# Performance work log

Hardware: AMD Instinct MI355X
Metric: run time of the kernel (lower is better)

The kernel has to match this reference:

```python
import jax, jax.numpy as jnp
import numpy as np

N_NODES = 100000
N_EDGES = 3200000
F_IN, F_HID, F_OUT = 32, 32, 16


def spline_conv(x, edge_index, edge_attr, W, root, bias):
    """SplineConv, dim=1, kernel_size=2, degree=1, open spline, aggr='mean'.
    Basis weights over the 2 kernel slots are (1-u, u) for pseudo u in [0,1).
    W: [2, Fin, Fout], root: [Fin, Fout], bias: [Fout]."""
    src, dst = edge_index[0], edge_index[1]
    u = jnp.clip(edge_attr[:, 0:1], 0.0, 1.0)          # [E,1]
    x_src = x[src]                                      # [E,Fin] gather
    msg = (1.0 - u) * (x_src @ W[0]) + u * (x_src @ W[1])  # [E,Fout]
    agg = jax.ops.segment_sum(msg, dst, num_segments=x.shape[0])
    cnt = jax.ops.segment_sum(jnp.ones((msg.shape[0],), dtype=x.dtype), dst,
                              num_segments=x.shape[0])
    agg = agg / jnp.maximum(cnt, 1.0)[:, None]          # mean aggregation
    return agg + x @ root + bias


def setup_inputs() -> dict:
    key = jax.random.key(0)
    ks = jax.random.split(key, 9)
    x = jax.random.normal(ks[0], (N_NODES, F_IN), dtype=jnp.float32)
    edge_index = jax.random.randint(ks[1], (2, N_EDGES), 0, N_NODES, dtype=jnp.int64)
    edge_attr = jax.random.uniform(ks[2], (N_EDGES, 1), dtype=jnp.float32)
    s1 = 1.0 / np.sqrt(F_IN)
    s2 = 1.0 / np.sqrt(F_HID)
    W1 = jax.random.normal(ks[3], (2, F_IN, F_HID), dtype=jnp.float32) * s1
    root1 = jax.random.normal(ks[4], (F_IN, F_HID), dtype=jnp.float32) * s1
    b1 = jnp.zeros((F_HID,), dtype=jnp.float32)
    W2 = jax.random.normal(ks[5], (2, F_HID, F_OUT), dtype=jnp.float32) * s2
    root2 = jax.random.normal(ks[6], (F_HID, F_OUT), dtype=jnp.float32) * s2
    b2 = jnp.zeros((F_OUT,), dtype=jnp.float32)
    return {"x": x, "edge_index": edge_index, "edge_attr": edge_attr,
            "W1": W1, "root1": root1, "b1": b1,
            "W2": W2, "root2": root2, "b2": b2}


def reference(x, edge_index, edge_attr, W1, root1, b1, W2, root2, b2):
    # dropout is identity in eval mode
    h = jax.nn.relu(spline_conv(x, edge_index, edge_attr, W1, root1, b1))
    h = spline_conv(h, edge_index, edge_attr, W2, root2, b2)
    return jax.nn.log_softmax(h, axis=1)
```

## Files before the change

### kernel.cpp

```cpp
#include <hip/hip_runtime.h>
#include <math.h>

#define NN 100000
#define NE 3200000
#define BSH 6
#define BSZ 64
#define NBKT 1563
#define CAP 2560
#define STILE 8192
#define NTBS 391
#define NPB 1563
#define TST 68
#define NOFF (NBKT + 1)
#define OS2W 392

#define FMA4(a, s, v) { (a).x += (s)*(v).x; (a).y += (s)*(v).y; (a).z += (s)*(v).z; (a).w += (s)*(v).w; }

typedef float v2f __attribute__((ext_vector_type(2)));

__device__ __forceinline__ unsigned fp8pack4(float a, float b, float c, float d) {
    int r = __builtin_amdgcn_cvt_pk_fp8_f32(a, b, 0, false);
    r = __builtin_amdgcn_cvt_pk_fp8_f32(c, d, r, true);
    return (unsigned)r;
}

#define LDE(pp, vv, idx) { int e_ = (idx); \
    if (e_ < cn) { pp = (unsigned)pks[cs + e_]; vv = x1[(size_t)(pp >> 15) * 8 + j]; } \
    else { pp = 0u; vv = 0u; } }
#define ACC(pp, vv) { float u_ = (float)((pp) & 511u) * (1.f / 511.f); \
    v2f lo_ = __builtin_amdgcn_cvt_pk_f32_fp8((vv), false); \
    v2f hi_ = __builtin_amdgcn_cvt_pk_f32_fp8((vv), true); \
    T0 += lo_.x; B0 += u_ * lo_.x;  T1 += lo_.y; B1 += u_ * lo_.y; \
    T2 += hi_.x; B2 += u_ * hi_.x;  T3 += hi_.y; B3 += u_ * hi_.y; }

__global__ __launch_bounds__(512, 6) void sp_k(
    const int* __restrict__ ei, const float* __restrict__ ea,
    const float* __restrict__ x, const float* __restrict__ R, const float* __restrict__ b,
    int* __restrict__ pk, unsigned short* __restrict__ offs,
    unsigned* __restrict__ xb, float* __restrict__ xr)
{
    __shared__ __align__(16) union {
        struct { int h[2048]; int staged[STILE]; } sc;
        struct { float Rs[1024]; float xs[64 * 33]; } pp;
    } sm;
    int t = threadIdx.x;

    if (blockIdx.x < NTBS) {
        int* h = sm.sc.h;
        for (int i = t; i < 2048; i += 512) h[i] = 0;
        __syncthreads();
        int e0 = blockIdx.x * STILE;
        int cntblk = NE - e0; if (cntblk > STILE) cntblk = STILE;
        unsigned pck[16]; int bk[16];
        #pragma unroll
        for (int i = 0; i < 16; i++) {
            int e = e0 + i * 512 + t;
            bk[i] = -1;
            if (e < NE) {
                int s = ei[e];
                int d = ei[NE + e];
                float u = fminf(fmaxf(ea[e], 0.f), 1.f);
                unsigned uq = __float2uint_rn(u * 511.f);
                bk[i] = d >> BSH;
                pck[i] = ((unsigned)s << 15) | ((unsigned)(d & (BSZ - 1)) << 9) | uq;
                atomicAdd(&h[bk[i]], 1);
            }
        }
        __syncthreads();
        int4 hc = ((const int4*)h)[t];
        int s4 = hc.x + hc.y + hc.z + hc.w;
        int lane = t & 63, wv = t >> 6;
        int inc = s4;
        #pragma unroll
        for (int ofs = 1; ofs < 64; ofs <<= 1) {
            int v = __shfl_up(inc, ofs);
            if (lane >= ofs) inc += v;
        }
        int* wsum = sm.sc.staged;
        if (lane == 63) wsum[wv] = inc;
        __syncthreads();
        int base = 0;
        #pragma unroll
        for (int i = 0; i < 8; i++) { int v = wsum[i]; if (i < wv) base += v; }
        int ex = base + inc - s4;
        ((int4*)h)[t] = make_int4(ex, ex + hc.x, ex + hc.x + hc.y, ex + hc.x + hc.y + hc.z);
        __syncthreads();
        for (int k = t; k < NOFF; k += 512)
            offs[(size_t)blockIdx.x * NOFF + k] = (unsigned short)h[k];
        __syncthreads();
        #pragma unroll
        for (int i = 0; i < 16; i++) {
            if (bk[i] >= 0) {
                int pos = atomicAdd(&h[bk[i]], 1);
                sm.sc.staged[pos] = (int)pck[i];
            }
        }
        __syncthreads();
        int* seg = pk + (size_t)blockIdx.x * STILE;
        for (int i = t; i * 4 < cntblk; i += 512)
            ((int4*)seg)[i] = ((const int4*)sm.sc.staged)[i];
    } else {
        for (int i = t; i < 1024; i += 512) sm.pp.Rs[i] = R[i];
        int nb = (blockIdx.x - NTBS) * 64;
        for (int i = t; i < 2048; i += 512) {
            int n = nb + (i >> 5);
            sm.pp.xs[(i >> 5) * 33 + (i & 31)] = (n < NN) ? x[n * 32 + (i & 31)] : 0.f;
        }
        __syncthreads();
        int local = t >> 3, c = t & 7;
        int n = nb + local;
        float4 a2 = make_float4(0.f, 0.f, 0.f, 0.f);
        #pragma unroll
        for (int k = 0; k < 32; k++) {
            float xk = sm.pp.xs[local * 33 + k];
            float4 r = ((const float4*)sm.pp.Rs)[k * 8 + c];
            FMA4(a2, xk, r);
        }
        if (n < NN) {
            float4 bb = ((const float4*)b)[c];
            a2.x += bb.x; a2.y += bb.y; a2.z += bb.z; a2.w += bb.w;
            ((float4*)xr)[n * 8 + c] = a2;
            xb[n * 8 + c] = fp8pack4(sm.pp.xs[local * 33 + c * 4 + 0],
                                     sm.pp.xs[local * 33 + c * 4 + 1],
                                     sm.pp.xs[local * 33 + c * 4 + 2],
                                     sm.pp.xs[local * 33 + c * 4 + 3]);
        }
    }
}

__global__ __launch_bounds__(256) void tr_k(
    const unsigned short* __restrict__ offs, unsigned* __restrict__ offs2)
{
    __shared__ unsigned short st[64][68];
    int kt = blockIdx.x % 25;
    int tt = blockIdx.x / 25;
    int t = threadIdx.x;
    for (int i = t; i < 64 * 66; i += 256) {
        int r = i / 66, c = i % 66;
        int row = tt * 64 + r, k = kt * 64 + c;
        st[r][c] = (row < NTBS && k < NOFF) ? offs[(size_t)row * NOFF + k] : (unsigned short)0;
    }
    __syncthreads();
    for (int i = t; i < 64 * 64; i += 256) {
        int kl = i >> 6, tl = i & 63;
        int k = kt * 64 + kl, row = tt * 64 + tl;
        if (k < NBKT && row < NTBS) {
            unsigned o0 = st[tl][kl];
            unsigned cnt = (unsigned)st[tl][kl + 1] - o0;
            offs2[(size_t)k * OS2W + row] = o0 | (cnt << 16);
        }
    }
}

__global__ __launch_bounds__(512, 6) void agg1_k(
    const int* __restrict__ pk, const unsigned* __restrict__ offs2,
    const unsigned* __restrict__ xb, const float* __restrict__ W,
    const float* __restrict__ R2, const float* __restrict__ b2,
    const float* __restrict__ xr, unsigned* __restrict__ hb, float* __restrict__ hr,
    int* __restrict__ pk2, int* __restrict__ cnt2)
{
    __shared__ float Wc[2048];
    __shared__ float R2s[512];
    __shared__ int ccnt[BSZ], coff[BSZ];
    __shared__ int wsum[8];
    __shared__ __align__(16) char smraw[BSZ * TST * 4];
    __shared__ __align__(16) union { int staged[CAP]; float hs[BSZ * 33]; } su;
    int* pks = (int*)smraw;
    float* tb = (float*)smraw;

    int t = threadIdx.x;
    for (int i = t; i < 1024; i += 512) {
        float w0 = W[i];
        Wc[i] = w0;
        Wc[1024 + i] = W[1024 + i] - w0;
    }
    if (t < 512) R2s[t] = R2[t];
    if (t < BSZ) ccnt[t] = 0;

    int bkt = blockIdx.x;
    int cnt = 0, o0 = 0;
    if (t < NTBS) {
        unsigned pc = offs2[(size_t)bkt * OS2W + t];
        o0 = (int)(pc & 0xFFFFu);
        cnt = (int)(pc >> 16);
    }
    int lane = t & 63, wv = t >> 6;
    int inc = cnt;
    #pragma unroll
    for (int ofs = 1; ofs < 64; ofs <<= 1) {
        int v = __shfl_up(inc, ofs);
        if (lane >= ofs) inc += v;
    }
    if (lane == 63) wsum[wv] = inc;
    __syncthreads();
    int base = 0, tot = 0;
    #pragma unroll
    for (int i = 0; i < 8; i++) { int v = wsum[i]; tot += v; if (i < wv) base += v; }
    int dst = base + inc - cnt;
    int ne = tot < CAP ? tot : CAP;
    if (dst + cnt > CAP) { cnt = CAP - dst; if (cnt < 0) cnt = 0; }
    const int* seg = pk + (size_t)t * STILE + o0;
    int i2 = 0;
    for (; i2 + 4 <= cnt; i2 += 4) {
        int v0 = seg[i2], v1 = seg[i2 + 1], v2 = seg[i2 + 2], v3 = seg[i2 + 3];
        su.staged[dst + i2] = v0; su.staged[dst + i2 + 1] = v1;
        su.staged[dst + i2 + 2] = v2; su.staged[dst + i2 + 3] = v3;
    }
    for (; i2 < cnt; i2++) su.staged[dst + i2] = seg[i2];
    __syncthreads();

    unsigned er[5]; int rk[5];
    #pragma unroll
    for (int i = 0; i < 5; i++) {
        int e = i * 512 + t;
        rk[i] = -1;
        if (e < ne) {
            er[i] = (unsigned)su.staged[e];
            rk[i] = atomicAdd(&ccnt[(er[i] >> 9) & (BSZ - 1)], 1);
        }
    }
    __syncthreads();
    if (t < BSZ) {
        int v = ccnt[t], sc = v;
        #pragma unroll
        for (int ofs = 1; ofs < 64; ofs <<= 1) {
            int nn = __shfl_up(sc, ofs);
            if (t >= ofs) sc += nn;
        }
        coff[t] = sc - v;
    }
    __syncthreads();
    #pragma unroll
    for (int i = 0; i < 5; i++)
        if (rk[i] >= 0) pks[coff[(er[i] >> 9) & (BSZ - 1)] + rk[i]] = (int)er[i];
    if (t < BSZ) cnt2[bkt * BSZ + t] = ccnt[t];
    __syncthreads();

    {
        int n4 = (ne + 3) >> 2;
        int4* dp = (int4*)(pk2 + (size_t)bkt * CAP);
        for (int i = t; i < n4; i += 512) dp[i] = ((const int4*)pks)[i];
    }

    int r = t >> 3, j = t & 7;
    int cs = coff[r], cn = ccnt[r];
    const unsigned* x1 = xb;
    float T0=0,T1=0,T2=0,T3=0,B0=0,B1=0,B2=0,B3=0;
    unsigned pa0, pa1, pa2, pa3, pb0, pb1, pb2, pb3;
    unsigned va0, va1, va2, va3, vb0, vb1, vb2, vb3;
    LDE(pa0, va0, 0) LDE(pa1, va1, 1) LDE(pa2, va2, 2) LDE(pa3, va3, 3)
    LDE(pb0, vb0, 4) LDE(pb1, vb1, 5) LDE(pb2, vb2, 6) LDE(pb3, vb3, 7)
    for (int k = 0; k < cn; k += 8) {
        ACC(pa0, va0) ACC(pa1, va1) ACC(pa2, va2) ACC(pa3, va3)
        LDE(pa0, va0, k + 8)  LDE(pa1, va1, k + 9)  LDE(pa2, va2, k + 10) LDE(pa3, va3, k + 11)
        ACC(pb0, vb0) ACC(pb1, vb1) ACC(pb2, vb2) ACC(pb3, vb3)
        LDE(pb0, vb0, k + 12) LDE(pb1, vb1, k + 13) LDE(pb2, vb2, k + 14) LDE(pb3, vb3, k + 15)
    }
    __syncthreads();

    ((float4*)(tb + r * TST + 4 * j))[0]      = make_float4(T0, T1, T2, T3);
    ((float4*)(tb + r * TST + 32 + 4 * j))[0] = make_float4(B0, B1, B2, B3);
    __syncthreads();

    {
        int row = t >> 3, cc = t & 7;
        int n = bkt * BSZ + row;
        float inv = 1.f / fmaxf((float)ccnt[row], 1.f);
        float4 acc = make_float4(0.f, 0.f, 0.f, 0.f);
        #pragma unroll
        for (int k = 0; k < 32; k++) {
            float sa = tb[row * TST + k];
            float4 w = ((const float4*)Wc)[k * 8 + cc];
            FMA4(acc, sa, w);
        }
        #pragma unroll
        for (int k = 0; k < 32; k++) {
            float sb = tb[row * TST + 32 + k];
            float4 w = ((const float4*)Wc)[(32 + k) * 8 + cc];
            FMA4(acc, sb, w);
        }
        float h0 = 0.f, h1 = 0.f, h2 = 0.f, h3 = 0.f;
        if (n < NN) {
            float4 rr = ((const float4*)xr)[n * 8 + cc];
            h0 = fmaxf(acc.x * inv + rr.x, 0.f);
            h1 = fmaxf(acc.y * inv + rr.y, 0.f);
            h2 = fmaxf(acc.z * inv + rr.z, 0.f);
            h3 = fmaxf(acc.w * inv + rr.w, 0.f);
            hb[n * 8 + cc] = fp8pack4(h0, h1, h2, h3);
        }
        su.hs[row * 33 + cc * 4 + 0] = h0;
        su.hs[row * 33 + cc * 4 + 1] = h1;
        su.hs[row * 33 + cc * 4 + 2] = h2;
        su.hs[row * 33 + cc * 4 + 3] = h3;
    }
    __syncthreads();

    #pragma unroll
    for (int p = 0; p < 2; p++) {
        int idx = p * 512 + t;
        int row = idx >> 4, f = idx & 15;
        int n = bkt * BSZ + row;
        if (n < NN) {
            float o = 0.f;
            #pragma unroll
            for (int k = 0; k < 32; k++) o += su.hs[row * 33 + k] * R2s[k * 16 + f];
            hr[n * 16 + f] = o + b2[f];
        }
    }
}

__global__ __launch_bounds__(512, 8) void agg2_k(
    const int* __restrict__ pk2, const int* __restrict__ cnt2,
    const unsigned* __restrict__ hb, const float* __restrict__ W,
    const float* __restrict__ hr, float* __restrict__ out)
{
    __shared__ float Wc[1024];
    __shared__ int ccnt[BSZ], coff[BSZ];
    __shared__ int smne;
    __shared__ __align__(16) char smraw[BSZ * TST * 4];
    int* pks = (int*)smraw;
    float* tb = (float*)smraw;

    int t = threadIdx.x;
    if (t < 512) {
        float w0 = W[t];
        Wc[t] = w0;
        Wc[512 + t] = W[512 + t] - w0;
    }
    int bkt = blockIdx.x;
    if (t < BSZ) {
        int v = cnt2[bkt * BSZ + t];
        ccnt[t] = v;
        int sc = v;
        #pragma unroll
        for (int ofs = 1; ofs < 64; ofs <<= 1) {
            int nn = __shfl_up(sc, ofs);
            if (t >= ofs) sc += nn;
        }
        coff[t] = sc - v;
        if (t == 63) smne = sc;
    }
    __syncthreads();
    int ne = smne; if (ne > CAP) ne = CAP;
    {
        int n4 = (ne + 3) >> 2;
        const int4* sp4 = (const int4*)(pk2 + (size_t)bkt * CAP);
        for (int i = t; i < n4; i += 512) ((int4*)pks)[i] = sp4[i];
    }
    __syncthreads();

    int r = t >> 3, j = t & 7;
    int cs = coff[r], cn = ccnt[r];
    const unsigned* x1 = hb;
    float T0=0,T1=0,T2=0,T3=0,B0=0,B1=0,B2=0,B3=0;
    unsigned pa0, pa1, pa2, pa3, pb0, pb1, pb2, pb3;
    unsigned va0, va1, va2, va3, vb0, vb1, vb2, vb3;
    LDE(pa0, va0, 0) LDE(pa1, va1, 1) LDE(pa2, va2, 2) LDE(pa3, va3, 3)
    LDE(pb0, vb0, 4) LDE(pb1, vb1, 5) LDE(pb2, vb2, 6) LDE(pb3, vb3, 7)
    for (int k = 0; k < cn; k += 8) {
        ACC(pa0, va0) ACC(pa1, va1) ACC(pa2, va2) ACC(pa3, va3)
        LDE(pa0, va0, k + 8)  LDE(pa1, va1, k + 9)  LDE(pa2, va2, k + 10) LDE(pa3, va3, k + 11)
        ACC(pb0, vb0) ACC(pb1, vb1) ACC(pb2, vb2) ACC(pb3, vb3)
        LDE(pb0, vb0, k + 12) LDE(pb1, vb1, k + 13) LDE(pb2, vb2, k + 14) LDE(pb3, vb3, k + 15)
    }
    __syncthreads();

    ((float4*)(tb + r * TST + 4 * j))[0]      = make_float4(T0, T1, T2, T3);
    ((float4*)(tb + r * TST + 32 + 4 * j))[0] = make_float4(B0, B1, B2, B3);
    __syncthreads();

    #pragma unroll
    for (int p = 0; p < 2; p++) {
        int row = p * 32 + (t >> 4), f = t & 15;
        int n = bkt * BSZ + row;
        float inv = 1.f / fmaxf((float)ccnt[row], 1.f);
        float o = 0.f;
        #pragma unroll
        for (int k = 0; k < 32; k++) o += tb[row * TST + k] * Wc[k * 16 + f];
        #pragma unroll
        for (int k = 0; k < 32; k++) o += tb[row * TST + 32 + k] * Wc[(32 + k) * 16 + f];
        if (n < NN) {
            o = o * inv + hr[n * 16 + f];
            float m = o;
            #pragma unroll
            for (int ofs = 8; ofs; ofs >>= 1) m = fmaxf(m, __shfl_xor(m, ofs, 16));
            float sm = expf(o - m);
            #pragma unroll
            for (int ofs = 8; ofs; ofs >>= 1) sm += __shfl_xor(sm, ofs, 16);
            out[n * 16 + f] = o - (m + logf(sm));
        }
    }
}

extern "C" void kernel_launch(void* const* d_in, const int* in_sizes, int n_in,
                              void* d_out, int out_size, void* d_ws, size_t ws_size,
                              hipStream_t stream) {
    const float* x     = (const float*)d_in[0];
    const int*   ei    = (const int*)d_in[1];
    const float* ea    = (const float*)d_in[2];
    const float* W1    = (const float*)d_in[3];
    const float* root1 = (const float*)d_in[4];
    const float* b1    = (const float*)d_in[5];
    const float* W2    = (const float*)d_in[6];
    const float* root2 = (const float*)d_in[7];
    const float* b2    = (const float*)d_in[8];
    float* out = (float*)d_out;

    int* ws = (int*)d_ws;
    int* pk = ws;
    size_t o_offs  = NE;
    size_t o_offs2 = o_offs + 305764;
    size_t o_pk2   = o_offs2 + (size_t)NBKT * OS2W;
    size_t o_cnt2  = o_pk2 + (size_t)NBKT * CAP;
    size_t o_xb    = o_cnt2 + (size_t)NBKT * BSZ;
    size_t o_hb    = o_xb + (size_t)NN * 8;
    size_t o_xr    = o_hb + (size_t)NN * 8;
    size_t o_hr    = o_xr + (size_t)NN * 32;

    unsigned short* offs = (unsigned short*)(ws + o_offs);
    unsigned* offs2 = (unsigned*)(ws + o_offs2);
    int* pk2 = ws + o_pk2;
    int* cnt2 = ws + o_cnt2;
    unsigned* xb = (unsigned*)(ws + o_xb);
    unsigned* hb = (unsigned*)(ws + o_hb);
    float* xr = (float*)(ws + o_xr);
    float* hr = (float*)(ws + o_hr);

    sp_k   <<<NTBS + NPB, 512, 0, stream>>>(ei, ea, x, root1, b1, pk, offs, xb, xr);
    tr_k   <<<25 * 7, 256, 0, stream>>>(offs, offs2);
    agg1_k <<<NBKT, 512, 0, stream>>>(pk, offs2, xb, W1, root2, b2, xr, hb, hr, pk2, cnt2);
    agg2_k <<<NBKT, 512, 0, stream>>>(pk2, cnt2, hb, W2, hr, out);
}
```

Measured before the change: 226.6 us.

## Split edge bucketing into two-level radix pass with dedicated partition kernel

```diff
diff --git a/kernel.cpp b/kernel.cpp
--- a/kernel.cpp
+++ b/kernel.cpp
@@ -3,16 +3,18 @@
 
 #define NN 100000
 #define NE 3200000
-#define BSH 6
 #define BSZ 64
 #define NBKT 1563
+#define NBKT2 1564
 #define CAP 2560
 #define STILE 8192
 #define NTBS 391
 #define NPB 1563
 #define TST 68
-#define NOFF (NBKT + 1)
-#define OS2W 392
+#define NSUP 391
+#define NOFA (NSUP + 1)
+#define OSBW 392
+#define SCAP 9216
 
 #define FMA4(a, s, v) { (a).x += (s)*(v).x; (a).y += (s)*(v).y; (a).z += (s)*(v).z; (a).w += (s)*(v).w; }
 
@@ -33,72 +35,95 @@
     T0 += lo_.x; B0 += u_ * lo_.x;  T1 += lo_.y; B1 += u_ * lo_.y; \
     T2 += hi_.x; B2 += u_ * hi_.x;  T3 += hi_.y; B3 += u_ * hi_.y; }
 
+#define WALK_BODY() \
+    int r = t >> 3, j = t & 7; \
+    int cs = coff[r], cn = ccnt[r]; \
+    float T0=0,T1=0,T2=0,T3=0,B0=0,B1=0,B2=0,B3=0; \
+    unsigned pa0, pa1, pa2, pa3, pb0, pb1, pb2, pb3; \
+    unsigned va0, va1, va2, va3, vb0, vb1, vb2, vb3; \
+    LDE(pa0, va0, 0) LDE(pa1, va1, 1) LDE(pa2, va2, 2) LDE(pa3, va3, 3) \
+    LDE(pb0, vb0, 4) LDE(pb1, vb1, 5) LDE(pb2, vb2, 6) LDE(pb3, vb3, 7) \
+    for (int k = 0; k < cn; k += 8) { \
+        ACC(pa0, va0) ACC(pa1, va1) ACC(pa2, va2) ACC(pa3, va3) \
+        LDE(pa0, va0, k + 8)  LDE(pa1, va1, k + 9)  LDE(pa2, va2, k + 10) LDE(pa3, va3, k + 11) \
+        ACC(pb0, vb0) ACC(pb1, vb1) ACC(pb2, vb2) ACC(pb3, vb3) \
+        LDE(pb0, vb0, k + 12) LDE(pb1, vb1, k + 13) LDE(pb2, vb2, k + 14) LDE(pb3, vb3, k + 15) \
+    } \
+    __syncthreads();                       \
+    ((float4*)(tb + r * TST + 4 * j))[0]      = make_float4(T0, T1, T2, T3); \
+    ((float4*)(tb + r * TST + 32 + 4 * j))[0] = make_float4(B0, B1, B2, B3); \
+    __syncthreads();
+
 __global__ __launch_bounds__(512, 6) void sp_k(
     const int* __restrict__ ei, const float* __restrict__ ea,
     const float* __restrict__ x, const float* __restrict__ R, const float* __restrict__ b,
-    int* __restrict__ pk, unsigned short* __restrict__ offs,
+    int* __restrict__ pkA, unsigned char* __restrict__ idxA, unsigned short* __restrict__ offsA,
     unsigned* __restrict__ xb, float* __restrict__ xr)
 {
     __shared__ __align__(16) union {
-        struct { int h[2048]; int staged[STILE]; } sc;
+        struct { int h[NSUP + 1]; int wsum[8]; int staged[STILE]; char sidx[STILE]; } sc;
         struct { float Rs[1024]; float xs[64 * 33]; } pp;
     } sm;
     int t = threadIdx.x;
 
     if (blockIdx.x < NTBS) {
         int* h = sm.sc.h;
-        for (int i = t; i < 2048; i += 512) h[i] = 0;
+        if (t < NSUP) h[t] = 0;
         __syncthreads();
         int e0 = blockIdx.x * STILE;
         int cntblk = NE - e0; if (cntblk > STILE) cntblk = STILE;
-        unsigned pck[16]; int bk[16];
+        unsigned pck[16]; int key[16];
         #pragma unroll
         for (int i = 0; i < 16; i++) {
             int e = e0 + i * 512 + t;
-            bk[i] = -1;
+            key[i] = -1;
             if (e < NE) {
                 int s = ei[e];
                 int d = ei[NE + e];
                 float u = fminf(fmaxf(ea[e], 0.f), 1.f);
                 unsigned uq = __float2uint_rn(u * 511.f);
-                bk[i] = d >> BSH;
-                pck[i] = ((unsigned)s << 15) | ((unsigned)(d & (BSZ - 1)) << 9) | uq;
-                atomicAdd(&h[bk[i]], 1);
+                key[i] = d >> 6;
+                pck[i] = ((unsigned)s << 15) | ((unsigned)(d & 63) << 9) | uq;
+                atomicAdd(&h[key[i] >> 2], 1);
             }
         }
         __syncthreads();
-        int4 hc = ((const int4*)h)[t];
-        int s4 = hc.x + hc.y + hc.z + hc.w;
+        int cb = (t < NSUP) ? h[t] : 0;
         int lane = t & 63, wv = t >> 6;
-        int inc = s4;
+        int inc = cb;
         #pragma unroll
         for (int ofs = 1; ofs < 64; ofs <<= 1) {
             int v = __shfl_up(inc, ofs);
             if (lane >= ofs) inc += v;
         }
-        int* wsum = sm.sc.staged;
-        if (lane == 63) wsum[wv] = inc;
+        if (lane == 63) sm.sc.wsum[wv] = inc;
         __syncthreads();
         int base = 0;
         #pragma unroll
-        for (int i = 0; i < 8; i++) { int v = wsum[i]; if (i < wv) base += v; }
-        int ex = base + inc - s4;
-        ((int4*)h)[t] = make_int4(ex, ex + hc.x, ex + hc.x + hc.y, ex + hc.x + hc.y + hc.z);
-        __syncthreads();
-        for (int k = t; k < NOFF; k += 512)
-            offs[(size_t)blockIdx.x * NOFF + k] = (unsigned short)h[k];
+        for (int i = 0; i < 8; i++) { int v = sm.sc.wsum[i]; if (i < wv) base += v; }
+        int ex = base + inc - cb;
+        __syncthreads();
+        if (t < NSUP) {
+            h[t] = ex;
+            offsA[(size_t)blockIdx.x * NOFA + t] = (unsigned short)ex;
+        }
+        if (t == 0) offsA[(size_t)blockIdx.x * NOFA + NSUP] = (unsigned short)cntblk;
         __syncthreads();
         #pragma unroll
         for (int i = 0; i < 16; i++) {
-            if (bk[i] >= 0) {
-                int pos = atomicAdd(&h[bk[i]], 1);
+            if (key[i] >= 0) {
+                int pos = atomicAdd(&h[key[i] >> 2], 1);
                 sm.sc.staged[pos] = (int)pck[i];
+                sm.sc.sidx[pos] = (char)(key[i] & 3);
             }
         }
         __syncthreads();
-        int* seg = pk + (size_t)blockIdx.x * STILE;
+        int* segA = pkA + (size_t)blockIdx.x * STILE;
         for (int i = t; i * 4 < cntblk; i += 512)
-            ((int4*)seg)[i] = ((const int4*)sm.sc.staged)[i];
+            ((int4*)segA)[i] = ((const int4*)sm.sc.staged)[i];
+        int4* segI = (int4*)(idxA + (size_t)blockIdx.x * STILE);
+        for (int i = t; i * 16 < cntblk; i += 512)
+            segI[i] = ((const int4*)sm.sc.sidx)[i];
     } else {
         for (int i = t; i < 1024; i += 512) sm.pp.Rs[i] = R[i];
         int nb = (blockIdx.x - NTBS) * 64;
@@ -129,42 +154,108 @@
 }
 
 __global__ __launch_bounds__(256) void tr_k(
-    const unsigned short* __restrict__ offs, unsigned* __restrict__ offs2)
+    const unsigned short* __restrict__ offsA, unsigned* __restrict__ offsB)
 {
     __shared__ unsigned short st[64][68];
-    int kt = blockIdx.x % 25;
-    int tt = blockIdx.x / 25;
+    int kt = blockIdx.x % 7;
+    int tt = blockIdx.x / 7;
     int t = threadIdx.x;
     for (int i = t; i < 64 * 66; i += 256) {
         int r = i / 66, c = i % 66;
         int row = tt * 64 + r, k = kt * 64 + c;
-        st[r][c] = (row < NTBS && k < NOFF) ? offs[(size_t)row * NOFF + k] : (unsigned short)0;
+        st[r][c] = (row < NTBS && k < NOFA) ? offsA[(size_t)row * NOFA + k] : (unsigned short)0;
     }
     __syncthreads();
     for (int i = t; i < 64 * 64; i += 256) {
         int kl = i >> 6, tl = i & 63;
-        int k = kt * 64 + kl, row = tt * 64 + tl;
-        if (k < NBKT && row < NTBS) {
+        int s = kt * 64 + kl, row = tt * 64 + tl;
+        if (s < NSUP && row < NTBS) {
             unsigned o0 = st[tl][kl];
             unsigned cnt = (unsigned)st[tl][kl + 1] - o0;
-            offs2[(size_t)k * OS2W + row] = o0 | (cnt << 16);
+            offsB[(size_t)s * OSBW + row] = o0 | (cnt << 16);
+        }
+    }
+}
+
+__global__ __launch_bounds__(512, 6) void pb_k(
+    const int* __restrict__ pkA, const unsigned char* __restrict__ idxA,
+    const unsigned* __restrict__ offsB,
+    int* __restrict__ pk2, int* __restrict__ cnt2)
+{
+    __shared__ int hist[256], cur[256], off[257], wsumB[8];
+    __shared__ __align__(16) int stagedB[SCAP];
+    int t = threadIdx.x;
+    int s = blockIdx.x;
+
+    int o0 = 0, cnt = 0;
+    if (t < NTBS) {
+        unsigned pc = offsB[(size_t)s * OSBW + t];
+        o0 = (int)(pc & 0xFFFFu);
+        cnt = (int)(pc >> 16);
+    }
+    if (t < 256) hist[t] = 0;
+    __syncthreads();
+
+    const int* segR = pkA + (size_t)t * STILE + o0;
+    const unsigned char* segI = idxA + (size_t)t * STILE + o0;
+    for (int i = 0; i < cnt; i++) {
+        int d9 = (int)segI[i] * 64 + ((segR[i] >> 9) & 63);
+        atomicAdd(&hist[d9], 1);
+    }
+    __syncthreads();
+
+    int cb = (t < 256) ? hist[t] : 0;
+    int lane = t & 63, wv = t >> 6;
+    int inc = cb;
+    #pragma unroll
+    for (int ofs = 1; ofs < 64; ofs <<= 1) {
+        int v = __shfl_up(inc, ofs);
+        if (lane >= ofs) inc += v;
+    }
+    if (lane == 63) wsumB[wv] = inc;
+    __syncthreads();
+    int base = 0;
+    #pragma unroll
+    for (int i = 0; i < 8; i++) { int v = wsumB[i]; if (i < wv) base += v; }
+    int ex = base + inc - cb;
+    if (t < 256) { off[t] = ex; cur[t] = ex; }
+    if (t == 255) off[256] = ex + cb;
+    __syncthreads();
+
+    for (int i = 0; i < cnt; i++) {
+        int rrec = segR[i];
+        int d9 = (int)segI[i] * 64 + ((rrec >> 9) & 63);
+        int pos = atomicAdd(&cur[d9], 1);
+        if (pos < SCAP) stagedB[pos] = rrec;
+    }
+    __syncthreads();
+
+    if (t < 256) cnt2[((size_t)s * 4 + (t >> 6)) * 64 + (t & 63)] = hist[t];
+    #pragma unroll
+    for (int bq = 0; bq < 4; bq++) {
+        int bas = off[bq * 64];
+        int n = off[(bq + 1) * 64] - bas;
+        if (n > CAP) n = CAP;
+        int* dp = pk2 + (size_t)(s * 4 + bq) * CAP;
+        for (int i = t; i < n; i += 512) {
+            int p2 = bas + i;
+            if (p2 < SCAP) dp[i] = stagedB[p2];
         }
     }
 }
 
 __global__ __launch_bounds__(512, 6) void agg1_k(
-    const int* __restrict__ pk, const unsigned* __restrict__ offs2,
+    const int* __restrict__ pk2, const int* __restrict__ cnt2,
     const unsigned* __restrict__ xb, const float* __restrict__ W,
     const float* __restrict__ R2, const float* __restrict__ b2,
-    const float* __restrict__ xr, unsigned* __restrict__ hb, float* __restrict__ hr,
-    int* __restrict__ pk2, int* __restrict__ cnt2)
+    const float* __restrict__ xr, unsigned* __restrict__ hb, float* __restrict__ hr)
 {
     __shared__ float Wc[2048];
     __shared__ float R2s[512];
     __shared__ int ccnt[BSZ], coff[BSZ];
-    __shared__ int wsum[8];
+    __shared__ int smne;
     __shared__ __align__(16) char smraw[BSZ * TST * 4];
-    __shared__ __align__(16) union { int staged[CAP]; float hs[BSZ * 33]; } su;
+    __shared__ float hs[BSZ * 33];
     int* pks = (int*)smraw;
     float* tb = (float*)smraw;
 
@@ -175,92 +266,31 @@
         Wc[1024 + i] = W[1024 + i] - w0;
     }
     if (t < 512) R2s[t] = R2[t];
-    if (t < BSZ) ccnt[t] = 0;
 
     int bkt = blockIdx.x;
-    int cnt = 0, o0 = 0;
-    if (t < NTBS) {
-        unsigned pc = offs2[(size_t)bkt * OS2W + t];
-        o0 = (int)(pc & 0xFFFFu);
-        cnt = (int)(pc >> 16);
-    }
-    int lane = t & 63, wv = t >> 6;
-    int inc = cnt;
-    #pragma unroll
-    for (int ofs = 1; ofs < 64; ofs <<= 1) {
-        int v = __shfl_up(inc, ofs);
-        if (lane >= ofs) inc += v;
-    }
-    if (lane == 63) wsum[wv] = inc;
-    __syncthreads();
-    int base = 0, tot = 0;
-    #pragma unroll
-    for (int i = 0; i < 8; i++) { int v = wsum[i]; tot += v; if (i < wv) base += v; }
-    int dst = base + inc - cnt;
-    int ne = tot < CAP ? tot : CAP;
-    if (dst + cnt > CAP) { cnt = CAP - dst; if (cnt < 0) cnt = 0; }
-    const int* seg = pk + (size_t)t * STILE + o0;
-    int i2 = 0;
-    for (; i2 + 4 <= cnt; i2 += 4) {
-        int v0 = seg[i2], v1 = seg[i2 + 1], v2 = seg[i2 + 2], v3 = seg[i2 + 3];
-        su.staged[dst + i2] = v0; su.staged[dst + i2 + 1] = v1;
-        su.staged[dst + i2 + 2] = v2; su.staged[dst + i2 + 3] = v3;
-    }
-    for (; i2 < cnt; i2++) su.staged[dst + i2] = seg[i2];
-    __syncthreads();
-
-    unsigned er[5]; int rk[5];
-    #pragma unroll
-    for (int i = 0; i < 5; i++) {
-        int e = i * 512 + t;
-        rk[i] = -1;
-        if (e < ne) {
-            er[i] = (unsigned)su.staged[e];
-            rk[i] = atomicAdd(&ccnt[(er[i] >> 9) & (BSZ - 1)], 1);
-        }
-    }
-    __syncthreads();
     if (t < BSZ) {
-        int v = ccnt[t], sc = v;
+        int v = cnt2[bkt * BSZ + t];
+        ccnt[t] = v;
+        int sc = v;
         #pragma unroll
         for (int ofs = 1; ofs < 64; ofs <<= 1) {
             int nn = __shfl_up(sc, ofs);
             if (t >= ofs) sc += nn;
         }
         coff[t] = sc - v;
-    }
-    __syncthreads();
-    #pragma unroll
-    for (int i = 0; i < 5; i++)
-        if (rk[i] >= 0) pks[coff[(er[i] >> 9) & (BSZ - 1)] + rk[i]] = (int)er[i];
-    if (t < BSZ) cnt2[bkt * BSZ + t] = ccnt[t];
-    __syncthreads();
-
+        if (t == 63) smne = sc;
+    }
+    __syncthreads();
+    int ne = smne; if (ne > CAP) ne = CAP;
     {
         int n4 = (ne + 3) >> 2;
-        int4* dp = (int4*)(pk2 + (size_t)bkt * CAP);
-        for (int i = t; i < n4; i += 512) dp[i] = ((const int4*)pks)[i];
-    }
-
-    int r = t >> 3, j = t & 7;
-    int cs = coff[r], cn = ccnt[r];
+        const int4* sp4 = (const int4*)(pk2 + (size_t)bkt * CAP);
+        for (int i = t; i < n4; i += 512) ((int4*)pks)[i] = sp4[i];
+    }
+    __syncthreads();
+
     const unsigned* x1 = xb;
-    float T0=0,T1=0,T2=0,T3=0,B0=0,B1=0,B2=0,B3=0;
-    unsigned pa0, pa1, pa2, pa3, pb0, pb1, pb2, pb3;
-    unsigned va0, va1, va2, va3, vb0, vb1, vb2, vb3;
-    LDE(pa0, va0, 0) LDE(pa1, va1, 1) LDE(pa2, va2, 2) LDE(pa3, va3, 3)
-    LDE(pb0, vb0, 4) LDE(pb1, vb1, 5) LDE(pb2, vb2, 6) LDE(pb3, vb3, 7)
-    for (int k = 0; k < cn; k += 8) {
-        ACC(pa0, va0) ACC(pa1, va1) ACC(pa2, va2) ACC(pa3, va3)
-        LDE(pa0, va0, k + 8)  LDE(pa1, va1, k + 9)  LDE(pa2, va2, k + 10) LDE(pa3, va3, k + 11)
-        ACC(pb0, vb0) ACC(pb1, vb1) ACC(pb2, vb2) ACC(pb3, vb3)
-        LDE(pb0, vb0, k + 12) LDE(pb1, vb1, k + 13) LDE(pb2, vb2, k + 14) LDE(pb3, vb3, k + 15)
-    }
-    __syncthreads();
-
-    ((float4*)(tb + r * TST + 4 * j))[0]      = make_float4(T0, T1, T2, T3);
-    ((float4*)(tb + r * TST + 32 + 4 * j))[0] = make_float4(B0, B1, B2, B3);
-    __syncthreads();
+    WALK_BODY()
 
     {
         int row = t >> 3, cc = t & 7;
@@ -288,10 +318,10 @@
             h3 = fmaxf(acc.w * inv + rr.w, 0.f);
             hb[n * 8 + cc] = fp8pack4(h0, h1, h2, h3);
         }
-        su.hs[row * 33 + cc * 4 + 0] = h0;
-        su.hs[row * 33 + cc * 4 + 1] = h1;
-        su.hs[row * 33 + cc * 4 + 2] = h2;
-        su.hs[row * 33 + cc * 4 + 3] = h3;
+        hs[row * 33 + cc * 4 + 0] = h0;
+        hs[row * 33 + cc * 4 + 1] = h1;
+        hs[row * 33 + cc * 4 + 2] = h2;
+        hs[row * 33 + cc * 4 + 3] = h3;
     }
     __syncthreads();
 
@@ -303,13 +333,13 @@
         if (n < NN) {
             float o = 0.f;
             #pragma unroll
-            for (int k = 0; k < 32; k++) o += su.hs[row * 33 + k] * R2s[k * 16 + f];
+            for (int k = 0; k < 32; k++) o += hs[row * 33 + k] * R2s[k * 16 + f];
             hr[n * 16 + f] = o + b2[f];
         }
     }
 }
 
-__global__ __launch_bounds__(512, 8) void agg2_k(
+__global__ __launch_bounds__(512, 6) void agg2_k(
     const int* __restrict__ pk2, const int* __restrict__ cnt2,
     const unsigned* __restrict__ hb, const float* __restrict__ W,
     const float* __restrict__ hr, float* __restrict__ out)
@@ -349,25 +379,8 @@
     }
     __syncthreads();
 
-    int r = t >> 3, j = t & 7;
-    int cs = coff[r], cn = ccnt[r];
     const unsigned* x1 = hb;
-    float T0=0,T1=0,T2=0,T3=0,B0=0,B1=0,B2=0,B3=0;
-    unsigned pa0, pa1, pa2, pa3, pb0, pb1, pb2, pb3;
-    unsigned va0, va1, va2, va3, vb0, vb1, vb2, vb3;
-    LDE(pa0, va0, 0) LDE(pa1, va1, 1) LDE(pa2, va2, 2) LDE(pa3, va3, 3)
-    LDE(pb0, vb0, 4) LDE(pb1, vb1, 5) LDE(pb2, vb2, 6) LDE(pb3, vb3, 7)
-    for (int k = 0; k < cn; k += 8) {
-        ACC(pa0, va0) ACC(pa1, va1) ACC(pa2, va2) ACC(pa3, va3)
-        LDE(pa0, va0, k + 8)  LDE(pa1, va1, k + 9)  LDE(pa2, va2, k + 10) LDE(pa3, va3, k + 11)
-        ACC(pb0, vb0) ACC(pb1, vb1) ACC(pb2, vb2) ACC(pb3, vb3)
-        LDE(pb0, vb0, k + 12) LDE(pb1, vb1, k + 13) LDE(pb2, vb2, k + 14) LDE(pb3, vb3, k + 15)
-    }
-    __syncthreads();
-
-    ((float4*)(tb + r * TST + 4 * j))[0]      = make_float4(T0, T1, T2, T3);
-    ((float4*)(tb + r * TST + 32 + 4 * j))[0] = make_float4(B0, B1, B2, B3);
-    __syncthreads();
+    WALK_BODY()
 
     #pragma unroll
     for (int p = 0; p < 2; p++) {
@@ -407,18 +420,21 @@
     float* out = (float*)d_out;
 
     int* ws = (int*)d_ws;
-    int* pk = ws;
-    size_t o_offs  = NE;
-    size_t o_offs2 = o_offs + 305764;
-    size_t o_pk2   = o_offs2 + (size_t)NBKT * OS2W;
-    size_t o_cnt2  = o_pk2 + (size_t)NBKT * CAP;
-    size_t o_xb    = o_cnt2 + (size_t)NBKT * BSZ;
+    size_t o_pkA   = 0;
+    size_t o_idxA  = o_pkA + (size_t)NTBS * STILE;
+    size_t o_offsA = o_idxA + (size_t)NTBS * STILE / 4;
+    size_t o_offsB = o_offsA + 76640;
+    size_t o_pk2   = o_offsB + (size_t)NSUP * OSBW;
+    size_t o_cnt2  = o_pk2 + (size_t)NBKT2 * CAP;
+    size_t o_xb    = o_cnt2 + (size_t)NBKT2 * 64;
     size_t o_hb    = o_xb + (size_t)NN * 8;
     size_t o_xr    = o_hb + (size_t)NN * 8;
     size_t o_hr    = o_xr + (size_t)NN * 32;
 
-    unsigned short* offs = (unsigned short*)(ws + o_offs);
-    unsigned* offs2 = (unsigned*)(ws + o_offs2);
+    int* pkA = ws + o_pkA;
+    unsigned char* idxA = (unsigned char*)(ws + o_idxA);
+    unsigned short* offsA = (unsigned short*)(ws + o_offsA);
+    unsigned* offsB = (unsigned*)(ws + o_offsB);
     int* pk2 = ws + o_pk2;
     int* cnt2 = ws + o_cnt2;
     unsigned* xb = (unsigned*)(ws + o_xb);
@@ -426,8 +442,9 @@
     float* xr = (float*)(ws + o_xr);
     float* hr = (float*)(ws + o_hr);
 
-    sp_k   <<<NTBS + NPB, 512, 0, stream>>>(ei, ea, x, root1, b1, pk, offs, xb, xr);
-    tr_k   <<<25 * 7, 256, 0, stream>>>(offs, offs2);
-    agg1_k <<<NBKT, 512, 0, stream>>>(pk, offs2, xb, W1, root2, b2, xr, hb, hr, pk2, cnt2);
+    sp_k   <<<NTBS + NPB, 512, 0, stream>>>(ei, ea, x, root1, b1, pkA, idxA, offsA, xb, xr);
+    tr_k   <<<49, 256, 0, stream>>>(offsA, offsB);
+    pb_k   <<<NSUP, 512, 0, stream>>>(pkA, idxA, offsB, pk2, cnt2);
+    agg1_k <<<NBKT, 512, 0, stream>>>(pk2, cnt2, xb, W1, root2, b2, xr, hb, hr);
     agg2_k <<<NBKT, 512, 0, stream>>>(pk2, cnt2, hb, W2, hr, out);
 }
```

Result: slower. 263.8 us (+16.4%).

## Split bucket sort out of agg1 into separate kernel and reuse scatter ranks

Applied to the files above, without the earlier changes.

```diff
diff --git a/kernel.cpp b/kernel.cpp
--- a/kernel.cpp
+++ b/kernel.cpp
@@ -33,6 +33,25 @@
     T0 += lo_.x; B0 += u_ * lo_.x;  T1 += lo_.y; B1 += u_ * lo_.y; \
     T2 += hi_.x; B2 += u_ * hi_.x;  T3 += hi_.y; B3 += u_ * hi_.y; }
 
+#define WALK_BODY() \
+    int r = t >> 3, j = t & 7; \
+    int cs = coff[r], cn = ccnt[r]; \
+    float T0=0,T1=0,T2=0,T3=0,B0=0,B1=0,B2=0,B3=0; \
+    unsigned pa0, pa1, pa2, pa3, pb0, pb1, pb2, pb3; \
+    unsigned va0, va1, va2, va3, vb0, vb1, vb2, vb3; \
+    LDE(pa0, va0, 0) LDE(pa1, va1, 1) LDE(pa2, va2, 2) LDE(pa3, va3, 3) \
+    LDE(pb0, vb0, 4) LDE(pb1, vb1, 5) LDE(pb2, vb2, 6) LDE(pb3, vb3, 7) \
+    for (int k = 0; k < cn; k += 8) { \
+        ACC(pa0, va0) ACC(pa1, va1) ACC(pa2, va2) ACC(pa3, va3) \
+        LDE(pa0, va0, k + 8)  LDE(pa1, va1, k + 9)  LDE(pa2, va2, k + 10) LDE(pa3, va3, k + 11) \
+        ACC(pb0, vb0) ACC(pb1, vb1) ACC(pb2, vb2) ACC(pb3, vb3) \
+        LDE(pb0, vb0, k + 12) LDE(pb1, vb1, k + 13) LDE(pb2, vb2, k + 14) LDE(pb3, vb3, k + 15) \
+    } \
+    __syncthreads();                       \
+    ((float4*)(tb + r * TST + 4 * j))[0]      = make_float4(T0, T1, T2, T3); \
+    ((float4*)(tb + r * TST + 32 + 4 * j))[0] = make_float4(B0, B1, B2, B3); \
+    __syncthreads();
+
 __global__ __launch_bounds__(512, 6) void sp_k(
     const int* __restrict__ ei, const float* __restrict__ ea,
     const float* __restrict__ x, const float* __restrict__ R, const float* __restrict__ b,
@@ -51,7 +70,7 @@
         __syncthreads();
         int e0 = blockIdx.x * STILE;
         int cntblk = NE - e0; if (cntblk > STILE) cntblk = STILE;
-        unsigned pck[16]; int bk[16];
+        unsigned pck[16]; int bk[16], rk[16];
         #pragma unroll
         for (int i = 0; i < 16; i++) {
             int e = e0 + i * 512 + t;
@@ -63,7 +82,7 @@
                 unsigned uq = __float2uint_rn(u * 511.f);
                 bk[i] = d >> BSH;
                 pck[i] = ((unsigned)s << 15) | ((unsigned)(d & (BSZ - 1)) << 9) | uq;
-                atomicAdd(&h[bk[i]], 1);
+                rk[i] = atomicAdd(&h[bk[i]], 1);
             }
         }
         __syncthreads();
@@ -83,18 +102,15 @@
         #pragma unroll
         for (int i = 0; i < 8; i++) { int v = wsum[i]; if (i < wv) base += v; }
         int ex = base + inc - s4;
+        __syncthreads();
         ((int4*)h)[t] = make_int4(ex, ex + hc.x, ex + hc.x + hc.y, ex + hc.x + hc.y + hc.z);
         __syncthreads();
         for (int k = t; k < NOFF; k += 512)
             offs[(size_t)blockIdx.x * NOFF + k] = (unsigned short)h[k];
         __syncthreads();
         #pragma unroll
-        for (int i = 0; i < 16; i++) {
-            if (bk[i] >= 0) {
-                int pos = atomicAdd(&h[bk[i]], 1);
-                sm.sc.staged[pos] = (int)pck[i];
-            }
-        }
+        for (int i = 0; i < 16; i++)
+            if (bk[i] >= 0) sm.sc.staged[h[bk[i]] + rk[i]] = (int)pck[i];
         __syncthreads();
         int* seg = pk + (size_t)blockIdx.x * STILE;
         for (int i = t; i * 4 < cntblk; i += 512)
@@ -152,32 +168,17 @@
     }
 }
 
-__global__ __launch_bounds__(512, 6) void agg1_k(
+__global__ __launch_bounds__(512, 8) void srt_k(
     const int* __restrict__ pk, const unsigned* __restrict__ offs2,
-    const unsigned* __restrict__ xb, const float* __restrict__ W,
-    const float* __restrict__ R2, const float* __restrict__ b2,
-    const float* __restrict__ xr, unsigned* __restrict__ hb, float* __restrict__ hr,
     int* __restrict__ pk2, int* __restrict__ cnt2)
 {
-    __shared__ float Wc[2048];
-    __shared__ float R2s[512];
-    __shared__ int ccnt[BSZ], coff[BSZ];
-    __shared__ int wsum[8];
-    __shared__ __align__(16) char smraw[BSZ * TST * 4];
-    __shared__ __align__(16) union { int staged[CAP]; float hs[BSZ * 33]; } su;
-    int* pks = (int*)smraw;
-    float* tb = (float*)smraw;
-
+    __shared__ int ccnt[BSZ], coff[BSZ], wsum[8];
+    __shared__ __align__(16) int staged[CAP];
+    __shared__ __align__(16) int pks[CAP];
     int t = threadIdx.x;
-    for (int i = t; i < 1024; i += 512) {
-        float w0 = W[i];
-        Wc[i] = w0;
-        Wc[1024 + i] = W[1024 + i] - w0;
-    }
-    if (t < 512) R2s[t] = R2[t];
+    int bkt = blockIdx.x;
     if (t < BSZ) ccnt[t] = 0;
 
-    int bkt = blockIdx.x;
     int cnt = 0, o0 = 0;
     if (t < NTBS) {
         unsigned pc = offs2[(size_t)bkt * OS2W + t];
@@ -203,10 +204,10 @@
     int i2 = 0;
     for (; i2 + 4 <= cnt; i2 += 4) {
         int v0 = seg[i2], v1 = seg[i2 + 1], v2 = seg[i2 + 2], v3 = seg[i2 + 3];
-        su.staged[dst + i2] = v0; su.staged[dst + i2 + 1] = v1;
-        su.staged[dst + i2 + 2] = v2; su.staged[dst + i2 + 3] = v3;
-    }
-    for (; i2 < cnt; i2++) su.staged[dst + i2] = seg[i2];
+        staged[dst + i2] = v0; staged[dst + i2 + 1] = v1;
+        staged[dst + i2 + 2] = v2; staged[dst + i2 + 3] = v3;
+    }
+    for (; i2 < cnt; i2++) staged[dst + i2] = seg[i2];
     __syncthreads();
 
     unsigned er[5]; int rk[5];
@@ -215,7 +216,7 @@
         int e = i * 512 + t;
         rk[i] = -1;
         if (e < ne) {
-            er[i] = (unsigned)su.staged[e];
+            er[i] = (unsigned)staged[e];
             rk[i] = atomicAdd(&ccnt[(er[i] >> 9) & (BSZ - 1)], 1);
         }
     }
@@ -236,31 +237,58 @@
     if (t < BSZ) cnt2[bkt * BSZ + t] = ccnt[t];
     __syncthreads();
 
+    int n4 = (ne + 3) >> 2;
+    int4* dp = (int4*)(pk2 + (size_t)bkt * CAP);
+    for (int i = t; i < n4; i += 512) dp[i] = ((const int4*)pks)[i];
+}
+
+__global__ __launch_bounds__(512, 8) void agg1_k(
+    const int* __restrict__ pk2, const int* __restrict__ cnt2,
+    const unsigned* __restrict__ xb, const float* __restrict__ W,
+    const float* __restrict__ R2, const float* __restrict__ b2,
+    const float* __restrict__ xr, unsigned* __restrict__ hb, float* __restrict__ hr)
+{
+    __shared__ float Wc[2048];
+    __shared__ float R2s[512];
+    __shared__ int ccnt[BSZ], coff[BSZ];
+    __shared__ int smne;
+    __shared__ __align__(16) char smraw[BSZ * TST * 4];
+    __shared__ float hs[BSZ * 33];
+    int* pks = (int*)smraw;
+    float* tb = (float*)smraw;
+
+    int t = threadIdx.x;
+    for (int i = t; i < 1024; i += 512) {
+        float w0 = W[i];
+        Wc[i] = w0;
+        Wc[1024 + i] = W[1024 + i] - w0;
+    }
+    if (t < 512) R2s[t] = R2[t];
+
+    int bkt = blockIdx.x;
+    if (t < BSZ) {
+        int v = cnt2[bkt * BSZ + t];
+        ccnt[t] = v;
+        int sc = v;
+        #pragma unroll
+        for (int ofs = 1; ofs < 64; ofs <<= 1) {
+            int nn = __shfl_up(sc, ofs);
+            if (t >= ofs) sc += nn;
+        }
+        coff[t] = sc - v;
+        if (t == 63) smne = sc;
+    }
+    __syncthreads();
+    int ne = smne; if (ne > CAP) ne = CAP;
     {
         int n4 = (ne + 3) >> 2;
-        int4* dp = (int4*)(pk2 + (size_t)bkt * CAP);
-        for (int i = t; i < n4; i += 512) dp[i] = ((const int4*)pks)[i];
-    }
-
-    int r = t >> 3, j = t & 7;
-    int cs = coff[r], cn = ccnt[r];
+        const int4* sp4 = (const int4*)(pk2 + (size_t)bkt * CAP);
+        for (int i = t; i < n4; i += 512) ((int4*)pks)[i] = sp4[i];
+    }
+    __syncthreads();
+
     const unsigned* x1 = xb;
-    float T0=0,T1=0,T2=0,T3=0,B0=0,B1=0,B2=0,B3=0;
-    unsigned pa0, pa1, pa2, pa3, pb0, pb1, pb2, pb3;
-    unsigned va0, va1, va2, va3, vb0, vb1, vb2, vb3;
-    LDE(pa0, va0, 0) LDE(pa1, va1, 1) LDE(pa2, va2, 2) LDE(pa3, va3, 3)
-    LDE(pb0, vb0, 4) LDE(pb1, vb1, 5) LDE(pb2, vb2, 6) LDE(pb3, vb3, 7)
-    for (int k = 0; k < cn; k += 8) {
-        ACC(pa0, va0) ACC(pa1, va1) ACC(pa2, va2) ACC(pa3, va3)
-        LDE(pa0, va0, k + 8)  LDE(pa1, va1, k + 9)  LDE(pa2, va2, k + 10) LDE(pa3, va3, k + 11)
-        ACC(pb0, vb0) ACC(pb1, vb1) ACC(pb2, vb2) ACC(pb3, vb3)
-        LDE(pb0, vb0, k + 12) LDE(pb1, vb1, k + 13) LDE(pb2, vb2, k + 14) LDE(pb3, vb3, k + 15)
-    }
-    __syncthreads();
-
-    ((float4*)(tb + r * TST + 4 * j))[0]      = make_float4(T0, T1, T2, T3);
-    ((float4*)(tb + r * TST + 32 + 4 * j))[0] = make_float4(B0, B1, B2, B3);
-    __syncthreads();
+    WALK_BODY()
 
     {
         int row = t >> 3, cc = t & 7;
@@ -288,10 +316,10 @@
             h3 = fmaxf(acc.w * inv + rr.w, 0.f);
             hb[n * 8 + cc] = fp8pack4(h0, h1, h2, h3);
         }
-        su.hs[row * 33 + cc * 4 + 0] = h0;
-        su.hs[row * 33 + cc * 4 + 1] = h1;
-        su.hs[row * 33 + cc * 4 + 2] = h2;
-        su.hs[row * 33 + cc * 4 + 3] = h3;
+        hs[row * 33 + cc * 4 + 0] = h0;
+        hs[row * 33 + cc * 4 + 1] = h1;
+        hs[row * 33 + cc * 4 + 2] = h2;
+        hs[row * 33 + cc * 4 + 3] = h3;
     }
     __syncthreads();
 
@@ -303,7 +331,7 @@
         if (n < NN) {
             float o = 0.f;
             #pragma unroll
-            for (int k = 0; k < 32; k++) o += su.hs[row * 33 + k] * R2s[k * 16 + f];
+            for (int k = 0; k < 32; k++) o += hs[row * 33 + k] * R2s[k * 16 + f];
             hr[n * 16 + f] = o + b2[f];
         }
     }
@@ -349,25 +377,8 @@
     }
     __syncthreads();
 
-    int r = t >> 3, j = t & 7;
-    int cs = coff[r], cn = ccnt[r];
     const unsigned* x1 = hb;
-    float T0=0,T1=0,T2=0,T3=0,B0=0,B1=0,B2=0,B3=0;
-    unsigned pa0, pa1, pa2, pa3, pb0, pb1, pb2, pb3;
-    unsigned va0, va1, va2, va3, vb0, vb1, vb2, vb3;
-    LDE(pa0, va0, 0) LDE(pa1, va1, 1) LDE(pa2, va2, 2) LDE(pa3, va3, 3)
-    LDE(pb0, vb0, 4) LDE(pb1, vb1, 5) LDE(pb2, vb2, 6) LDE(pb3, vb3, 7)
-    for (int k = 0; k < cn; k += 8) {
-        ACC(pa0, va0) ACC(pa1, va1) ACC(pa2, va2) ACC(pa3, va3)
-        LDE(pa0, va0, k + 8)  LDE(pa1, va1, k + 9)  LDE(pa2, va2, k + 10) LDE(pa3, va3, k + 11)
-        ACC(pb0, vb0) ACC(pb1, vb1) ACC(pb2, vb2) ACC(pb3, vb3)
-        LDE(pb0, vb0, k + 12) LDE(pb1, vb1, k + 13) LDE(pb2, vb2, k + 14) LDE(pb3, vb3, k + 15)
-    }
-    __syncthreads();
-
-    ((float4*)(tb + r * TST + 4 * j))[0]      = make_float4(T0, T1, T2, T3);
-    ((float4*)(tb + r * TST + 32 + 4 * j))[0] = make_float4(B0, B1, B2, B3);
-    __syncthreads();
+    WALK_BODY()
 
     #pragma unroll
     for (int p = 0; p < 2; p++) {
@@ -407,8 +418,8 @@
     float* out = (float*)d_out;
 
     int* ws = (int*)d_ws;
-    int* pk = ws;
-    size_t o_offs  = NE;
+    size_t o_pk    = 0;
+    size_t o_offs  = o_pk + (size_t)NTBS * STILE;
     size_t o_offs2 = o_offs + 305764;
     size_t o_pk2   = o_offs2 + (size_t)NBKT * OS2W;
     size_t o_cnt2  = o_pk2 + (size_t)NBKT * CAP;
@@ -417,6 +428,7 @@
     size_t o_xr    = o_hb + (size_t)NN * 8;
     size_t o_hr    = o_xr + (size_t)NN * 32;
 
+    int* pk = ws + o_pk;
     unsigned short* offs = (unsigned short*)(ws + o_offs);
     unsigned* offs2 = (unsigned*)(ws + o_offs2);
     int* pk2 = ws + o_pk2;
@@ -428,6 +440,7 @@
 
     sp_k   <<<NTBS + NPB, 512, 0, stream>>>(ei, ea, x, root1, b1, pk, offs, xb, xr);
     tr_k   <<<25 * 7, 256, 0, stream>>>(offs, offs2);
-    agg1_k <<<NBKT, 512, 0, stream>>>(pk, offs2, xb, W1, root2, b2, xr, hb, hr, pk2, cnt2);
+    srt_k  <<<NBKT, 512, 0, stream>>>(pk, offs2, pk2, cnt2);
+    agg1_k <<<NBKT, 512, 0, stream>>>(pk2, cnt2, xb, W1, root2, b2, xr, hb, hr);
     agg2_k <<<NBKT, 512, 0, stream>>>(pk2, cnt2, hb, W2, hr, out);
 }
```

Result: slower. 236.6 us (+4.4%).
